# Kernel optimization log

Hardware: AMD Instinct MI355X
Metric: run time of the kernel (lower is better)

## Reference

```python
import jax, jax.numpy as jnp
import numpy as np
from jax import lax

PI = 3.141592653
TWO_PI = 2.0 * PI
IOU_THR = 0.3


def limit_period(val):
    return val - jnp.floor(val / TWO_PI + 0.5) * TWO_PI


def box_corners_bev(b):
    # b: [7] = (x, y, z, dx, dy, dz, heading) -> [4,2] CCW BEV corners
    signs = jnp.array([[0.5, -0.5], [0.5, 0.5], [-0.5, 0.5], [-0.5, -0.5]], jnp.float32)
    local = signs * jnp.stack([b[3], b[4]])
    c, s = jnp.cos(b[6]), jnp.sin(b[6])
    rot_t = jnp.stack([jnp.stack([c, s]), jnp.stack([-s, c])])  # R^T
    return local @ rot_t + jnp.stack([b[0], b[1]])


def clip_halfplane(poly, cnt, a, b):
    # Sutherland-Hodgman: clip poly[:cnt] (CCW) by left side of edge a->b. Buffer V=8.
    V = poly.shape[0]
    idx = jnp.arange(V)
    nxt = jnp.where(idx + 1 < cnt, idx + 1, 0)
    p1, p2 = poly, poly[nxt]
    e = b - a
    d1 = e[0] * (p1[:, 1] - a[1]) - e[1] * (p1[:, 0] - a[0])
    d2 = e[0] * (p2[:, 1] - a[1]) - e[1] * (p2[:, 0] - a[0])
    in1, in2 = d1 >= 0, d2 >= 0
    valid = idx < cnt
    denom = d1 - d2
    t = d1 / jnp.where(jnp.abs(denom) > 1e-8, denom, 1.0)
    inter = p1 + t[:, None] * (p2 - p1)
    emit = jnp.stack([in1 & valid, (in1 ^ in2) & valid], 1).reshape(2 * V)
    vals = jnp.stack([p1, inter], 1).reshape(2 * V, 2)
    pos = jnp.cumsum(emit) - 1
    scatter_idx = jnp.where(emit, pos, 2 * V)  # out-of-range -> dropped
    new_poly = jnp.zeros((V, 2), poly.dtype).at[scatter_idx].set(vals, mode='drop')
    return new_poly, emit.sum().astype(jnp.int32)


def poly_area(poly, cnt):
    V = poly.shape[0]
    idx = jnp.arange(V)
    nxt = jnp.where(idx + 1 < cnt, idx + 1, 0)
    p2 = poly[nxt]
    cr = poly[:, 0] * p2[:, 1] - p2[:, 0] * poly[:, 1]
    return 0.5 * jnp.abs(jnp.sum(jnp.where(idx < cnt, cr, 0.0)))


def pair_iou3d(ba, bb):
    pa, pb = box_corners_bev(ba), box_corners_bev(bb)
    poly = jnp.zeros((8, 2), jnp.float32).at[:4].set(pa)
    cnt = jnp.int32(4)
    for k in range(4):
        poly, cnt = clip_halfplane(poly, cnt, pb[k], pb[(k + 1) % 4])
    inter_bev = poly_area(poly, cnt)
    top = jnp.minimum(ba[2] + 0.5 * ba[5], bb[2] + 0.5 * bb[5])
    bot = jnp.maximum(ba[2] - 0.5 * ba[5], bb[2] - 0.5 * bb[5])
    inter = inter_bev * jnp.maximum(top - bot, 0.0)
    va = ba[3] * ba[4] * ba[5]
    vb = bb[3] * bb[4] * bb[5]
    return inter / jnp.maximum(va + vb - inter, 1e-6)


def pairwise_iou3d(boxes):
    return jax.vmap(lambda a: jax.vmap(lambda b: pair_iou3d(a, b))(boxes))(boxes)


def clustering(ious):
    # Faithful port of the sequential while-loop: repeatedly take first unassigned
    # box and stamp everything with iou > 0.3 to the current cluster id.
    n = ious.shape[0]

    def body(i, carry):
        ci, cur = carry
        unassigned = ci == 0
        has = jnp.any(unassigned)
        first = jnp.argmax(unassigned)
        m = ious[first] > IOU_THR
        ci = jnp.where(has & m, cur, ci)
        return ci, cur + jnp.where(has, 1, 0).astype(jnp.int32)

    ci, _ = lax.fori_loop(0, n, body, (jnp.zeros(n, jnp.int32), jnp.int32(1)))
    return ci


def cluster_fusion(boxes, scores, cluster_indices):
    # Masked, vmapped version of per-cluster weighted circular-mean fusion.
    # Output row (cid-1) is the fused box for cluster cid; empty slots are zero.
    n = boxes.shape[0]

    def fuse_one(cid):
        mask = cluster_indices == cid
        valid = jnp.any(mask)
        s = jnp.where(mask, scores, 0.0)
        dirs = boxes[:, 6]
        d0 = dirs[jnp.argmax(jnp.where(mask, scores, -jnp.inf))]
        diff = jnp.abs(dirs - d0)
        diff = jnp.where(diff > PI, TWO_PI - diff, diff)
        gt = diff > PI / 2
        flip_gt = jnp.sum(s * gt) <= jnp.sum(s * (~gt))
        dirs = jnp.where(jnp.where(flip_gt, gt, ~gt), dirs + PI, dirs)
        dirs = limit_period(dirs)
        sn = s / jnp.where(valid, jnp.sum(s), 1.0)
        sint = jnp.where(valid, jnp.sum(jnp.sin(dirs) * sn), 0.0)
        cost = jnp.where(valid, jnp.sum(jnp.cos(dirs) * sn), 1.0)
        theta = jnp.arctan2(sint, cost)
        center_dim = jnp.sum(boxes[:, :6] * sn[:, None], axis=0)
        return jnp.where(valid, jnp.concatenate([center_dim, theta[None]]), 0.0)

    return jax.vmap(fuse_one)(jnp.arange(1, n + 1, dtype=jnp.int32))


def setup_inputs() -> dict:
    key = jax.random.key(0)
    k1, k2, k3, k4, k5, k6 = jax.random.split(key, 6)
    N, G = 1024, 256  # 1024 detections clustered around 256 locations
    anchors = jax.random.uniform(k1, (G, 2), minval=-60.0, maxval=60.0)
    xy = anchors[jnp.repeat(jnp.arange(G), N // G)] + 0.8 * jax.random.normal(k2, (N, 2))
    z = jax.random.uniform(k3, (N, 1), minval=-1.0, maxval=1.0)
    dims = jax.random.uniform(k4, (N, 3), minval=jnp.array([3.5, 1.5, 1.4]),
                              maxval=jnp.array([4.5, 2.0, 1.8]))
    heading = jax.random.uniform(k5, (N, 1), minval=-PI, maxval=PI)
    pred_boxes = jnp.concatenate([xy, z, dims, heading], axis=1).astype(jnp.float32)
    pred_scores = jax.random.uniform(k6, (N,), minval=0.1, maxval=1.0)
    return {"pred_boxes": pred_boxes, "pred_scores": pred_scores}


def reference(pred_boxes, pred_scores):
    boxes = pred_boxes.at[:, 6].set(limit_period(pred_boxes[:, 6]))
    ious = pairwise_iou3d(boxes)
    ci = clustering(ious)
    return cluster_fusion(boxes, pred_scores, ci)
```

## Files before the change

kernel.cpp:

```cpp
#include <hip/hip_runtime.h>
#include <math.h>

#define NBOX 1024
#define PI_F 3.141592653f
#define TWO_PI_F 6.283185306f
#define HALF_PI_F 1.5707963265f
#define IOU_THR_F 0.3f

__device__ __forceinline__ float limit_period_f(float v) {
    return v - floorf(v / TWO_PI_F + 0.5f) * TWO_PI_F;
}

__device__ __forceinline__ void clip_edge(float (&px)[8], float (&py)[8], int &cnt,
                                          float axp, float ayp, float bxp, float byp) {
    float ex = bxp - axp, ey = byp - ayp;
    float d[8];
#pragma unroll
    for (int v = 0; v < 8; ++v)
        d[v] = ex * (py[v] - ayp) - ey * (px[v] - axp);

    float cxv[16], cyv[16];
    bool fl[16];
#pragma unroll
    for (int v = 0; v < 8; ++v) {
        bool valid = v < cnt;
        bool wrap = !(v + 1 < cnt);
        float p2x = wrap ? px[0] : px[(v + 1) & 7];
        float p2y = wrap ? py[0] : py[(v + 1) & 7];
        float d2v = wrap ? d[0] : d[(v + 1) & 7];
        float d1v = d[v];
        bool in1 = d1v >= 0.0f, in2 = d2v >= 0.0f;
        fl[2 * v] = in1 && valid;
        cxv[2 * v] = px[v];
        cyv[2 * v] = py[v];
        fl[2 * v + 1] = (in1 != in2) && valid;
        float den = d1v - d2v;
        float t = d1v / (fabsf(den) > 1e-8f ? den : 1.0f);
        cxv[2 * v + 1] = px[v] + t * (p2x - px[v]);
        cyv[2 * v + 1] = py[v] + t * (p2y - py[v]);
    }

    int pos = 0;
    float ox[8], oy[8];
#pragma unroll
    for (int o = 0; o < 8; ++o) { ox[o] = 0.0f; oy[o] = 0.0f; }
#pragma unroll
    for (int c = 0; c < 16; ++c) {
#pragma unroll
        for (int o = 0; o < 8; ++o) {
            if (o > c) continue;
            if (fl[c] && pos == o) { ox[o] = cxv[c]; oy[o] = cyv[c]; }
        }
        pos += fl[c] ? 1 : 0;
    }
    cnt = pos > 8 ? 8 : pos;
#pragma unroll
    for (int v = 0; v < 8; ++v) { px[v] = ox[v]; py[v] = oy[v]; }
}

__global__ __launch_bounds__(256) void iou_adj_kernel(const float* __restrict__ boxes,
                                                      unsigned long long* __restrict__ adj) {
    int t = blockIdx.x * 256 + threadIdx.x;
    int i = t >> 10;
    int j = t & 1023;
    const float* ba = boxes + i * 7;
    const float* bb = boxes + j * 7;
    float ax = ba[0], ay = ba[1], az = ba[2], al = ba[3], aw = ba[4], ah = ba[5];
    float bx = bb[0], by = bb[1], bz = bb[2], bl = bb[3], bw = bb[4], bh = bb[5];
    float tha = limit_period_f(ba[6]);
    float thb = limit_period_f(bb[6]);

    bool hit = false;
    float dx = ax - bx, dy = ay - by;
    float ra = 0.5f * sqrtf(al * al + aw * aw);
    float rb = 0.5f * sqrtf(bl * bl + bw * bw);
    float top = fminf(az + 0.5f * ah, bz + 0.5f * bh);
    float bot = fmaxf(az - 0.5f * ah, bz - 0.5f * bh);
    float hov = fmaxf(top - bot, 0.0f);
    float rr = ra + rb;
    if (dx * dx + dy * dy <= rr * rr && hov > 0.0f) {
        float ca = cosf(tha), sa = sinf(tha);
        float cb = cosf(thb), sb = sinf(thb);

        float px[8], py[8];
        {
            float hx = 0.5f * al, hy = 0.5f * aw;
            float sxv[4] = { hx, hx, -hx, -hx };
            float syv[4] = { -hy, hy, hy, -hy };
#pragma unroll
            for (int k = 0; k < 4; ++k) {
                px[k] = sxv[k] * ca - syv[k] * sa + ax;
                py[k] = sxv[k] * sa + syv[k] * ca + ay;
            }
#pragma unroll
            for (int k = 4; k < 8; ++k) { px[k] = 0.0f; py[k] = 0.0f; }
        }
        float qx[4], qy[4];
        {
            float hx = 0.5f * bl, hy = 0.5f * bw;
            float sxv[4] = { hx, hx, -hx, -hx };
            float syv[4] = { -hy, hy, hy, -hy };
#pragma unroll
            for (int k = 0; k < 4; ++k) {
                qx[k] = sxv[k] * cb - syv[k] * sb + bx;
                qy[k] = sxv[k] * sb + syv[k] * cb + by;
            }
        }
        int cnt = 4;
#pragma unroll
        for (int k = 0; k < 4; ++k)
            clip_edge(px, py, cnt, qx[k], qy[k], qx[(k + 1) & 3], qy[(k + 1) & 3]);

        float s2 = 0.0f;
#pragma unroll
        for (int v = 0; v < 8; ++v) {
            bool valid = v < cnt;
            bool wrap = !(v + 1 < cnt);
            float p2x = wrap ? px[0] : px[(v + 1) & 7];
            float p2y = wrap ? py[0] : py[(v + 1) & 7];
            float cr = px[v] * p2y - p2x * py[v];
            s2 += valid ? cr : 0.0f;
        }
        float area = 0.5f * fabsf(s2);
        float inter = area * hov;
        float va = al * aw * ah, vb = bl * bw * bh;
        float iou = inter / fmaxf(va + vb - inter, 1e-6f);
        hit = iou > IOU_THR_F;
    }
    unsigned long long bal = __ballot(hit);
    if ((threadIdx.x & 63) == 0)
        adj[t >> 6] = bal;
}

__global__ __launch_bounds__(256) void transpose_kernel(const unsigned long long* __restrict__ adj,
                                                        unsigned short* __restrict__ T) {
    int row = (blockIdx.x * 256 + threadIdx.x) >> 6;
    row = __builtin_amdgcn_readfirstlane(row);
    int lane = threadIdx.x & 63;
    const unsigned long long* rp = adj + row * 16;
    unsigned int acc = 0;
#pragma unroll
    for (int k = 0; k < 16; ++k) {
        unsigned long long w = rp[k];
        acc |= (unsigned int)((w >> lane) & 1ull) << k;
    }
    T[row * 64 + lane] = (unsigned short)acc;
}

__global__ __launch_bounds__(1024) void cluster_kernel(const unsigned long long* __restrict__ T64,
                                                       int* __restrict__ ci,
                                                       int* __restrict__ nclust_out) {
    __shared__ unsigned long long sT64[NBOX * 16];
    __shared__ int sseq[NBOX];
    __shared__ int part[16][64];
    const unsigned short* sT = (const unsigned short*)sT64;
    int tid = threadIdx.x;
#pragma unroll
    for (int j = 0; j < 16; ++j)
        sT64[j * 1024 + tid] = T64[j * 1024 + tid];
    __syncthreads();

    int wid = tid >> 6;
    int lane = tid & 63;

    if (wid == 0) {
        unsigned int um = 0xFFFFu;
        int cur = 1;
        for (int tau = 0; tau < 16; ++tau) {
            unsigned short tb[64];
#pragma unroll
            for (int k = 0; k < 64; ++k)
                tb[k] = sT[(tau * 64 + k) * 64 + lane];
            int myseq = 0;
#pragma unroll
            for (int k = 0; k < 64; ++k) {
                int umk = __builtin_amdgcn_readlane((int)um, k);
                int sd = (umk >> tau) & 1;
                unsigned int m = (0u - (unsigned int)sd) & (unsigned int)tb[k];
                um &= ~m;
                int curv = cur & (-sd);
                cur += sd;
                myseq = (lane == k) ? curv : myseq;
            }
            sseq[tau * 64 + lane] = myseq;
        }
        if (lane == 0)
            *nclust_out = cur - 1;
    }
    __syncthreads();

    int c = 0;
    int rbase = wid * 64;
#pragma unroll 8
    for (int d = 0; d < 64; ++d) {
        int r = rbase + d;
        unsigned int t = sT[r * 64 + lane];
        int sq = sseq[r];
#pragma unroll
        for (int g = 0; g < 1; ++g) { }
        (void)t; (void)sq;
        break;
    }
    int cg[16];
#pragma unroll
    for (int g = 0; g < 16; ++g) cg[g] = 0;
#pragma unroll 4
    for (int d = 0; d < 64; ++d) {
        int r = rbase + d;
        unsigned int t = sT[r * 64 + lane];
        int sq = sseq[r];
#pragma unroll
        for (int g = 0; g < 16; ++g) {
            bool hitb = ((t >> g) & 1u) != 0u;
            cg[g] = (hitb && sq > cg[g]) ? sq : cg[g];
        }
    }
#pragma unroll
    for (int g = 0; g < 16; ++g) {
        part[wid][lane] = cg[g];
        __syncthreads();
        if (wid == 0) {
            int m = part[0][lane];
#pragma unroll
            for (int w = 1; w < 16; ++w) m = m > part[w][lane] ? m : part[w][lane];
            ci[g * 64 + lane] = m;
        }
        __syncthreads();
    }
}

__global__ __launch_bounds__(256) void fusion_kernel(const float* __restrict__ boxes,
                                                     const float* __restrict__ scores,
                                                     const int* __restrict__ ci,
                                                     const int* __restrict__ nclust_p,
                                                     float* __restrict__ out) {
    __shared__ float sb[NBOX][7];
    __shared__ float ss[NBOX];
    __shared__ int   sc[NBOX];
    int tid = threadIdx.x;
    int nclust = *nclust_p;

    if (blockIdx.x * 4 + 1 > nclust) {
        if (tid < 28) {
            out[blockIdx.x * 28 + tid] = 0.0f;
        }
        return;
    }

    for (int idx = tid; idx < NBOX * 7; idx += 256) {
        float v = boxes[idx];
        int col = idx % 7;
        if (col == 6) v = limit_period_f(v);
        sb[idx / 7][col] = v;
    }
    for (int b = tid; b < NBOX; b += 256) {
        ss[b] = scores[b];
        sc[b] = ci[b];
    }
    __syncthreads();

    int wave = tid >> 6;
    int lane = tid & 63;
    int cid = blockIdx.x * 4 + wave + 1;

    float bv = -INFINITY;
    int bi = 0;
    for (int c = 0; c < 16; ++c) {
        int b = c * 64 + lane;
        float v = (sc[b] == cid) ? ss[b] : -INFINITY;
        if (v > bv) { bv = v; bi = b; }
    }
#pragma unroll
    for (int off = 32; off > 0; off >>= 1) {
        float ov = __shfl_xor(bv, off);
        int   oi = __shfl_xor(bi, off);
        if (ov > bv || (ov == bv && oi < bi)) { bv = ov; bi = oi; }
    }
    float* o = out + (cid - 1) * 7;
    if (!(bv > -INFINITY)) {
        if (lane == 0) {
#pragma unroll
            for (int jj = 0; jj < 7; ++jj) o[jj] = 0.0f;
        }
        return;
    }
    float d0 = sb[bi][6];

    float sgt = 0.0f, sngt = 0.0f, ssum = 0.0f;
    for (int c = 0; c < 16; ++c) {
        int b = c * 64 + lane;
        float s = (sc[b] == cid) ? ss[b] : 0.0f;
        float diff = fabsf(sb[b][6] - d0);
        diff = (diff > PI_F) ? (TWO_PI_F - diff) : diff;
        bool gt = diff > HALF_PI_F;
        sgt += gt ? s : 0.0f;
        sngt += gt ? 0.0f : s;
        ssum += s;
    }
#pragma unroll
    for (int off = 32; off > 0; off >>= 1) {
        sgt  += __shfl_xor(sgt, off);
        sngt += __shfl_xor(sngt, off);
        ssum += __shfl_xor(ssum, off);
    }
    bool flip = (sgt <= sngt);
    float inv = ssum;

    float sint = 0.0f, cost = 0.0f;
    float acc[6] = { 0.0f, 0.0f, 0.0f, 0.0f, 0.0f, 0.0f };
    for (int c = 0; c < 16; ++c) {
        int b = c * 64 + lane;
        float s = (sc[b] == cid) ? ss[b] : 0.0f;
        float sn = s / inv;
        float dH = sb[b][6];
        float diff = fabsf(dH - d0);
        diff = (diff > PI_F) ? (TWO_PI_F - diff) : diff;
        bool gt = diff > HALF_PI_F;
        bool cond = flip ? gt : !gt;
        float dd = cond ? (dH + PI_F) : dH;
        dd = limit_period_f(dd);
        sint += sinf(dd) * sn;
        cost += cosf(dd) * sn;
#pragma unroll
        for (int jj = 0; jj < 6; ++jj)
            acc[jj] += sb[b][jj] * sn;
    }
#pragma unroll
    for (int off = 32; off > 0; off >>= 1) {
        sint += __shfl_xor(sint, off);
        cost += __shfl_xor(cost, off);
#pragma unroll
        for (int jj = 0; jj < 6; ++jj)
            acc[jj] += __shfl_xor(acc[jj], off);
    }

    if (lane == 0) {
#pragma unroll
        for (int jj = 0; jj < 6; ++jj) o[jj] = acc[jj];
        o[6] = atan2f(sint, cost);
    }
}

extern "C" void kernel_launch(void* const* d_in, const int* in_sizes, int n_in,
                              void* d_out, int out_size, void* d_ws, size_t ws_size,
                              hipStream_t stream) {
    const float* boxes  = (const float*)d_in[0];
    const float* scores = (const float*)d_in[1];
    unsigned long long* adj = (unsigned long long*)d_ws;
    unsigned short* T = (unsigned short*)((char*)d_ws + (size_t)NBOX * 16 * 8);
    int* ci     = (int*)d_ws;
    int* nclust = (int*)((char*)d_ws + 4096);
    float* out = (float*)d_out;

    iou_adj_kernel<<<(NBOX * NBOX) / 256, 256, 0, stream>>>(boxes, adj);
    transpose_kernel<<<NBOX / 4, 256, 0, stream>>>(adj, T);
    cluster_kernel<<<1, 1024, 0, stream>>>((const unsigned long long*)T, ci, nclust);
    fusion_kernel<<<NBOX / 4, 256, 0, stream>>>(boxes, scores, ci, nclust, out);
}
```

Baseline: 162.4 us.

## Drop transpose kernel and resolve clustering per 64-block with ffs-driven greedy loop

Removes the separate bit-transpose kernel and has the cluster kernel read the raw adjacency bitmask directly, reinterpreting it as 16-bit chunks. The serial greedy clustering loop changes from a fixed 64-step per-block scan to a while loop. That loop picks the next surviving seed with find-first-set, kills its in-block neighbours via the diagonal 64x64 block, and assigns sequence numbers with mbcnt ranks. This saves a launch and global round trip and shortens the serial critical path when a block has few seeds. It relies on the adjacency being symmetric and changes the ci output indexing to match the untransposed layout.

```diff
diff --git a/kernel.cpp b/kernel.cpp
--- a/kernel.cpp
+++ b/kernel.cpp
@@ -132,32 +132,17 @@
         adj[t >> 6] = bal;
 }
 
-__global__ __launch_bounds__(256) void transpose_kernel(const unsigned long long* __restrict__ adj,
-                                                        unsigned short* __restrict__ T) {
-    int row = (blockIdx.x * 256 + threadIdx.x) >> 6;
-    row = __builtin_amdgcn_readfirstlane(row);
-    int lane = threadIdx.x & 63;
-    const unsigned long long* rp = adj + row * 16;
-    unsigned int acc = 0;
-#pragma unroll
-    for (int k = 0; k < 16; ++k) {
-        unsigned long long w = rp[k];
-        acc |= (unsigned int)((w >> lane) & 1ull) << k;
-    }
-    T[row * 64 + lane] = (unsigned short)acc;
-}
-
-__global__ __launch_bounds__(1024) void cluster_kernel(const unsigned long long* __restrict__ T64,
+__global__ __launch_bounds__(1024) void cluster_kernel(const unsigned long long* __restrict__ adj,
                                                        int* __restrict__ ci,
                                                        int* __restrict__ nclust_out) {
-    __shared__ unsigned long long sT64[NBOX * 16];
+    __shared__ unsigned long long sA[NBOX * 16];
     __shared__ int sseq[NBOX];
     __shared__ int part[16][64];
-    const unsigned short* sT = (const unsigned short*)sT64;
+    const unsigned short* sA16 = (const unsigned short*)sA;
     int tid = threadIdx.x;
 #pragma unroll
     for (int j = 0; j < 16; ++j)
-        sT64[j * 1024 + tid] = T64[j * 1024 + tid];
+        sA[j * 1024 + tid] = adj[j * 1024 + tid];
     __syncthreads();
 
     int wid = tid >> 6;
@@ -166,53 +151,52 @@
     if (wid == 0) {
         unsigned int um = 0xFFFFu;
         int cur = 1;
-        for (int tau = 0; tau < 16; ++tau) {
-            unsigned short tb[64];
-#pragma unroll
-            for (int k = 0; k < 64; ++k)
-                tb[k] = sT[(tau * 64 + k) * 64 + lane];
-            int myseq = 0;
-#pragma unroll
-            for (int k = 0; k < 64; ++k) {
-                int umk = __builtin_amdgcn_readlane((int)um, k);
-                int sd = (umk >> tau) & 1;
-                unsigned int m = (0u - (unsigned int)sd) & (unsigned int)tb[k];
-                um &= ~m;
-                int curv = cur & (-sd);
-                cur += sd;
-                myseq = (lane == k) ? curv : myseq;
+        for (int t = 0; t < 16; ++t) {
+            unsigned long long dv = sA[(t * 64 + lane) * 16 + t];
+            unsigned int dlo = (unsigned int)dv;
+            unsigned int dhi = (unsigned int)(dv >> 32);
+            unsigned long long c =
+                ((unsigned long long)((unsigned int)__builtin_amdgcn_readlane((int)um, 4 * t)     & 0xFFFFu)) |
+                ((unsigned long long)((unsigned int)__builtin_amdgcn_readlane((int)um, 4 * t + 1) & 0xFFFFu) << 16) |
+                ((unsigned long long)((unsigned int)__builtin_amdgcn_readlane((int)um, 4 * t + 2) & 0xFFFFu) << 32) |
+                ((unsigned long long)((unsigned int)__builtin_amdgcn_readlane((int)um, 4 * t + 3) & 0xFFFFu) << 48);
+            unsigned long long M = 0ull;
+            unsigned int kill = 0u;
+            while (c) {
+                int s = __ffsll((long long)c) - 1;
+                unsigned long long Ws =
+                    ((unsigned long long)(unsigned int)__builtin_amdgcn_readlane((int)dhi, s) << 32) |
+                    (unsigned long long)(unsigned int)__builtin_amdgcn_readlane((int)dlo, s);
+                M |= (1ull << s);
+                c &= ~Ws;
+                c &= ~(1ull << s);
+                kill |= (unsigned int)sA16[(t * 64 + s) * 64 + lane];
             }
-            sseq[tau * 64 + lane] = myseq;
+            um &= ~kill;
+            unsigned int mlo = (unsigned int)M, mhi = (unsigned int)(M >> 32);
+            int rank = __builtin_amdgcn_mbcnt_hi(mhi, __builtin_amdgcn_mbcnt_lo(mlo, 0));
+            int sd = (int)((M >> lane) & 1ull);
+            sseq[t * 64 + lane] = sd ? (cur + rank) : 0;
+            cur += __builtin_popcountll(M);
         }
         if (lane == 0)
             *nclust_out = cur - 1;
     }
     __syncthreads();
 
-    int c = 0;
+    int cg[16];
+#pragma unroll
+    for (int g = 0; g < 16; ++g) cg[g] = 0;
     int rbase = wid * 64;
-#pragma unroll 8
-    for (int d = 0; d < 64; ++d) {
-        int r = rbase + d;
-        unsigned int t = sT[r * 64 + lane];
-        int sq = sseq[r];
-#pragma unroll
-        for (int g = 0; g < 1; ++g) { }
-        (void)t; (void)sq;
-        break;
-    }
-    int cg[16];
-#pragma unroll
-    for (int g = 0; g < 16; ++g) cg[g] = 0;
 #pragma unroll 4
     for (int d = 0; d < 64; ++d) {
         int r = rbase + d;
-        unsigned int t = sT[r * 64 + lane];
+        unsigned int x = sA16[r * 64 + lane];
         int sq = sseq[r];
 #pragma unroll
         for (int g = 0; g < 16; ++g) {
-            bool hitb = ((t >> g) & 1u) != 0u;
-            cg[g] = (hitb && sq > cg[g]) ? sq : cg[g];
+            bool h = ((x >> g) & 1u) != 0u;
+            cg[g] = (h && sq > cg[g]) ? sq : cg[g];
         }
     }
 #pragma unroll
@@ -223,7 +207,7 @@
             int m = part[0][lane];
 #pragma unroll
             for (int w = 1; w < 16; ++w) m = m > part[w][lane] ? m : part[w][lane];
-            ci[g * 64 + lane] = m;
+            ci[lane * 16 + g] = m;
         }
         __syncthreads();
     }
@@ -347,13 +331,11 @@
     const float* boxes  = (const float*)d_in[0];
     const float* scores = (const float*)d_in[1];
     unsigned long long* adj = (unsigned long long*)d_ws;
-    unsigned short* T = (unsigned short*)((char*)d_ws + (size_t)NBOX * 16 * 8);
     int* ci     = (int*)d_ws;
     int* nclust = (int*)((char*)d_ws + 4096);
     float* out = (float*)d_out;
 
     iou_adj_kernel<<<(NBOX * NBOX) / 256, 256, 0, stream>>>(boxes, adj);
-    transpose_kernel<<<NBOX / 4, 256, 0, stream>>>(adj, T);
-    cluster_kernel<<<1, 1024, 0, stream>>>((const unsigned long long*)T, ci, nclust);
+    cluster_kernel<<<1, 1024, 0, stream>>>(adj, ci, nclust);
     fusion_kernel<<<NBOX / 4, 256, 0, stream>>>(boxes, scores, ci, nclust, out);
 }
```

New measurement: 181.2 us. 1.12x slower.
